# Kernel optimization log

Hardware: AMD Instinct MI355X
Metric: run time of the kernel (lower is better)

Reference implementation:

```python
import jax, jax.numpy as jnp
import numpy as np

K = 15          # n_clusters
D = 64          # dim_latent
M = 100         # number of w samples
LOG_2PI = float(np.log(2.0 * np.pi))

# state -> (cluster A, cluster B) edge endpoints, upper-triangular incl. diagonal
_A, _B = np.nonzero(np.triu(np.ones((K, K))))  # each [S], S = K*(K+1)/2 = 120


def setup_inputs() -> dict:
    key = jax.random.key(0)
    k1, k2, k3 = jax.random.split(key, 3)
    z = jax.random.normal(k1, (4096, 1, D), dtype=jnp.float32)      # [B, L, D]
    pi = jax.random.normal(k2, (1, K * (K + 1) // 2), dtype=jnp.float32)  # [1, S]
    mu = jax.random.uniform(k3, (D, K), dtype=jnp.float32, minval=-1.0, maxval=1.0)
    return {"z": z, "pi": pi, "mu": mu}


def reference(z, pi, mu):
    # w grid: [M]
    w = jnp.arange(M, dtype=z.dtype) / M
    # interpolated component means mu_sm[d, s, m] = mu[d,A[s]]*w[m] + mu[d,B[s]]*(1-w[m])
    mu_sm = mu[:, _A, None] * w + mu[:, _B, None] * (1.0 - w)   # [D, S, M]
    log_pi = jnp.log(jax.nn.softmax(pi, axis=-1) + 1e-30)       # [1, S]

    # squared distance via ||z||^2 - 2 z.mu + ||mu||^2 (avoids [B,L,D,S,M] materialization)
    zz = jnp.sum(z * z, axis=-1)                                # [B, L]
    cross = jnp.einsum('bld,dsm->blsm', z, mu_sm)               # [B, L, S, M]
    mm = jnp.sum(mu_sm * mu_sm, axis=0)                         # [S, M]
    sq = zz[..., None, None] - 2.0 * cross + mm                 # [B, L, S, M]

    log_p_zc_w = (-0.5 * D * LOG_2PI
                  + log_pi[0][None, None, :, None]
                  - 0.5 * sq)                                   # [B, L, S, M]
    log_p_z_L = jax.scipy.special.logsumexp(log_p_zc_w, axis=(2, 3))  # [B, L]
    log_p_z = jnp.mean(log_p_z_L) - jnp.log(jnp.asarray(M, z.dtype))
    return log_p_z
```

## Files before the change

### kernel.cpp

```cpp
#include <hip/hip_runtime.h>
#include <math.h>
#include <float.h>

#define D 64
#define K 15
#define S 120
#define MNUM 100
#define C0 (-58.81206612509905f)
#define L2E 1.4426950408889634f
#define INV_L2E 0.6931471805599453f
#define LOGM 4.605170185988091f

static __device__ __forceinline__ float fexp2(float x) {
    return __builtin_amdgcn_exp2f(x);
}

__global__ __launch_bounds__(256) void gmm_fused(const float* __restrict__ z,
                                                 const float* __restrict__ pi,
                                                 const float* __restrict__ mu,
                                                 float* __restrict__ out) {
    __shared__ float mush[D * K];
    __shared__ float G0[S], G1[S], G2[S];
    __shared__ unsigned char iA[S], iB[S];
    __shared__ float zsh[4][D];
    __shared__ float red[4];
    __shared__ float bsum[4];

    const int t = threadIdx.x;
    const int lane = t & 63;
    const int wv = t >> 6;

    for (int i = t; i < D * K; i += 256) mush[i] = mu[i];

    float p = (t < S) ? pi[t] : -FLT_MAX;
    float mx = p;
    #pragma unroll
    for (int off = 32; off; off >>= 1) mx = fmaxf(mx, __shfl_xor(mx, off));
    if (lane == 0) red[wv] = mx;
    __syncthreads();
    mx = fmaxf(fmaxf(red[0], red[1]), fmaxf(red[2], red[3]));

    float e = (t < S) ? __expf(p - mx) : 0.f;
    float se = e;
    #pragma unroll
    for (int off = 32; off; off >>= 1) se += __shfl_xor(se, off);
    __syncthreads();
    if (lane == 0) red[wv] = se;
    __syncthreads();
    se = red[0] + red[1] + red[2] + red[3];

    if (t < S) {
        float sm = e / se;
        float logpi = logf(sm + 1e-30f);

        int i = 0, rem = t;
        while (rem >= K - i) { rem -= K - i; ++i; }
        int j = i + rem;

        float aa = 0.f, ab = 0.f, bb = 0.f;
        #pragma unroll 8
        for (int d = 0; d < D; ++d) {
            float ma = mush[d * K + i];
            float mb = mush[d * K + j];
            aa = fmaf(ma, ma, aa);
            ab = fmaf(ma, mb, ab);
            bb = fmaf(mb, mb, bb);
        }
        float q0 = bb;
        float q1 = 2.f * (ab - bb);
        float q2 = aa - 2.f * ab + bb;

        G0[t] = C0 + logpi - 0.5f * q0;
        G1[t] = -0.5f * q1;
        G2[t] = -0.5f * q2;
        iA[t] = (unsigned char)i;
        iB[t] = (unsigned char)j;
    }

    const int b = (blockIdx.x << 2) + wv;
    float zval = z[b * D + lane];
    zsh[wv][lane] = zval;
    float zz = zval * zval;
    #pragma unroll
    for (int off = 32; off; off >>= 1) zz += __shfl_xor(zz, off);
    __syncthreads();

    const int g = lane >> 4;
    const int kk = lane & 15;
    const int kkc = (kk < K) ? kk : (K - 1);
    const float* zw = &zsh[wv][g * 16];
    float cpart = 0.f;
    #pragma unroll
    for (int i = 0; i < 16; ++i)
        cpart = fmaf(zw[i], mush[(g * 16 + i) * K + kkc], cpart);
    cpart += __shfl_xor(cpart, 16);
    cpart += __shfl_xor(cpart, 32);

    const int s1 = lane;
    const int s2 = lane + 64;
    const bool v2 = (s2 < S);
    const int s2c = v2 ? s2 : (S - 1);

    float cA1 = __shfl(cpart, (int)iA[s1]);
    float cB1 = __shfl(cpart, (int)iB[s1]);
    float cA2 = __shfl(cpart, (int)iA[s2c]);
    float cB2 = __shfl(cpart, (int)iB[s2c]);

    float T01 = G0[s1] + cB1 - 0.5f * zz;
    float T11 = G1[s1] + (cA1 - cB1);
    float T21 = G2[s1];
    float T02 = v2 ? (G0[s2c] + cB2 - 0.5f * zz) : -1e30f;
    float T12 = G1[s2c] + (cA2 - cB2);
    float T22 = G2[s2c];

    float bnd = fmaxf(T01, fmaf(0.99f, fmaf(0.99f, T21, T11), T01));
    if (T21 < 0.f) {
        float wv1 = fminf(fmaxf(-T11 * 0.5f * __builtin_amdgcn_rcpf(T21), 0.f), 0.99f);
        bnd = fmaxf(bnd, fmaf(wv1, fmaf(wv1, T21, T11), T01));
    }
    if (v2) {
        float b2 = fmaxf(T02, fmaf(0.99f, fmaf(0.99f, T22, T12), T02));
        if (T22 < 0.f) {
            float wv2 = fminf(fmaxf(-T12 * 0.5f * __builtin_amdgcn_rcpf(T22), 0.f), 0.99f);
            b2 = fmaxf(b2, fmaf(wv2, fmaf(wv2, T22, T12), T02));
        }
        bnd = fmaxf(bnd, b2);
    }
    #pragma unroll
    for (int off = 32; off; off >>= 1) bnd = fmaxf(bnd, __shfl_xor(bnd, off));
    const float Mb = bnd;

    const float a01 = (T01 - Mb) * L2E, a11 = T11 * L2E, a21 = T21 * L2E;
    const float a02 = (T02 - Mb) * L2E, a12 = T12 * L2E, a22 = T22 * L2E;

    float e1  = fexp2(fmaf(0.5f, fmaf(0.5f, a21, a11), a01));
    float g1  = fexp2(fmaf(0.0101f, a21,  0.01f * a11));
    float dd1 = fexp2(fmaf(-0.0099f, a21, -0.01f * a11));
    float h1  = fexp2(2.0e-4f * a21);

    float e2  = fexp2(fmaf(0.5f, fmaf(0.5f, a22, a12), a02));
    float g2  = fexp2(fmaf(0.0101f, a22,  0.01f * a12));
    float dd2 = fexp2(fmaf(-0.0099f, a22, -0.01f * a12));
    float h2  = fexp2(2.0e-4f * a22);

    float eu1 = e1,        gu1 = g1;
    float ed1 = e1 * dd1,  du1 = dd1 * h1;
    float eu2 = e2,        gu2 = g2;
    float ed2 = e2 * dd2,  du2 = dd2 * h2;
    float su1 = 0.f, sd1 = 0.f, su2 = 0.f, sd2 = 0.f;

    #pragma unroll 10
    for (int m = 0; m < 50; ++m) {
        su1 += eu1; eu1 *= gu1; gu1 *= h1;
        sd1 += ed1; ed1 *= du1; du1 *= h1;
        su2 += eu2; eu2 *= gu2; gu2 *= h2;
        sd2 += ed2; ed2 *= du2; du2 *= h2;
    }

    float ssum = (su1 + sd1) + (su2 + sd2);
    #pragma unroll
    for (int off = 32; off; off >>= 1) ssum += __shfl_xor(ssum, off);

    if (lane == 0)
        bsum[wv] = Mb + __builtin_amdgcn_logf(ssum) * INV_L2E;
    __syncthreads();
    if (t == 0) {
        float blk = ((bsum[0] + bsum[1]) + (bsum[2] + bsum[3]) - 4.f * LOGM)
                    * (1.0f / 4096.0f);
        atomicAdd(out, blk);
    }
}

extern "C" void kernel_launch(void* const* d_in, const int* in_sizes, int n_in,
                              void* d_out, int out_size, void* d_ws, size_t ws_size,
                              hipStream_t stream) {
    const float* z  = (const float*)d_in[0];
    const float* pi = (const float*)d_in[1];
    const float* mu = (const float*)d_in[2];
    float* out = (float*)d_out;

    hipMemsetAsync(out, 0, sizeof(float), stream);
    gmm_fused<<<1024, 256, 0, stream>>>(z, pi, mu, out);
}
```

Baseline: 75.99 us.

## Process two batch rows per wavefront and halve grid size

```diff
diff --git a/kernel.cpp b/kernel.cpp
--- a/kernel.cpp
+++ b/kernel.cpp
@@ -11,8 +11,16 @@
 #define INV_L2E 0.6931471805599453f
 #define LOGM 4.605170185988091f
 
-static __device__ __forceinline__ float fexp2(float x) {
-    return __builtin_amdgcn_exp2f(x);
+static __device__ __forceinline__ float fexp2(float x) { return __builtin_amdgcn_exp2f(x); }
+static __device__ __forceinline__ float flog2(float x) { return __builtin_amdgcn_logf(x); }
+
+static __device__ __forceinline__ float qbound(float T0, float T1, float T2, float r2) {
+    float bnd = fmaxf(T0, fmaf(0.99f, fmaf(0.99f, T2, T1), T0));
+    if (T2 < 0.f) {
+        float wx = fminf(fmaxf(-T1 * 0.5f * r2, 0.f), 0.99f);
+        bnd = fmaxf(bnd, fmaf(wx, fmaf(wx, T2, T1), T0));
+    }
+    return bnd;
 }
 
 __global__ __launch_bounds__(256) void gmm_fused(const float* __restrict__ z,
@@ -21,152 +29,182 @@
                                                  float* __restrict__ out) {
     __shared__ float mush[D * K];
     __shared__ float G0[S], G1[S], G2[S];
-    __shared__ unsigned char iA[S], iB[S];
-    __shared__ float zsh[4][D];
-    __shared__ float red[4];
-    __shared__ float bsum[4];
+    __shared__ int   iA[S], iB[S];
+    __shared__ float zsh[8][D];
+    __shared__ float bsum[8];
 
     const int t = threadIdx.x;
     const int lane = t & 63;
     const int wv = t >> 6;
+    const int b0 = (blockIdx.x << 3) + (wv << 1);
+
+    float zv0 = z[b0 * D + lane];
+    float zv1 = z[b0 * D + D + lane];
 
     for (int i = t; i < D * K; i += 256) mush[i] = mu[i];
 
-    float p = (t < S) ? pi[t] : -FLT_MAX;
-    float mx = p;
-    #pragma unroll
-    for (int off = 32; off; off >>= 1) mx = fmaxf(mx, __shfl_xor(mx, off));
-    if (lane == 0) red[wv] = mx;
+    zsh[(wv << 1)][lane] = zv0;
+    zsh[(wv << 1) + 1][lane] = zv1;
+    float zz0 = zv0 * zv0, zz1 = zv1 * zv1;
+    #pragma unroll
+    for (int off = 32; off; off >>= 1) {
+        zz0 += __shfl_xor(zz0, off);
+        zz1 += __shfl_xor(zz1, off);
+    }
+
     __syncthreads();
-    mx = fmaxf(fmaxf(red[0], red[1]), fmaxf(red[2], red[3]));
-
-    float e = (t < S) ? __expf(p - mx) : 0.f;
-    float se = e;
-    #pragma unroll
-    for (int off = 32; off; off >>= 1) se += __shfl_xor(se, off);
+
+    if (t < 128) {
+        float pa = pi[lane];
+        float pb = (lane < S - 64) ? pi[lane + 64] : -FLT_MAX;
+        float mx = fmaxf(pa, pb);
+        #pragma unroll
+        for (int off = 32; off; off >>= 1) mx = fmaxf(mx, __shfl_xor(mx, off));
+        float ea = fexp2((pa - mx) * L2E);
+        float eb = (lane < S - 64) ? fexp2((pb - mx) * L2E) : 0.f;
+        float se = ea + eb;
+        #pragma unroll
+        for (int off = 32; off; off >>= 1) se += __shfl_xor(se, off);
+
+        if (t < S) {
+            float e = wv ? eb : ea;
+            float logpi = logf(e / se + 1e-30f);
+
+            int i = 0, rem = t;
+            while (rem >= K - i) { rem -= K - i; ++i; }
+            int j = i + rem;
+
+            float aa = 0.f, ab = 0.f, bb = 0.f;
+            #pragma unroll 8
+            for (int d = 0; d < D; ++d) {
+                float ma = mush[d * K + i];
+                float mb = mush[d * K + j];
+                aa = fmaf(ma, ma, aa);
+                ab = fmaf(ma, mb, ab);
+                bb = fmaf(mb, mb, bb);
+            }
+            float q0 = bb;
+            float q1 = 2.f * (ab - bb);
+            float q2 = aa - 2.f * ab + bb;
+
+            G0[t] = C0 + logpi - 0.5f * q0;
+            G1[t] = -0.5f * q1;
+            G2[t] = -0.5f * q2;
+            iA[t] = i;
+            iB[t] = j;
+        }
+    }
     __syncthreads();
-    if (lane == 0) red[wv] = se;
-    __syncthreads();
-    se = red[0] + red[1] + red[2] + red[3];
-
-    if (t < S) {
-        float sm = e / se;
-        float logpi = logf(sm + 1e-30f);
-
-        int i = 0, rem = t;
-        while (rem >= K - i) { rem -= K - i; ++i; }
-        int j = i + rem;
-
-        float aa = 0.f, ab = 0.f, bb = 0.f;
-        #pragma unroll 8
-        for (int d = 0; d < D; ++d) {
-            float ma = mush[d * K + i];
-            float mb = mush[d * K + j];
-            aa = fmaf(ma, ma, aa);
-            ab = fmaf(ma, mb, ab);
-            bb = fmaf(mb, mb, bb);
-        }
-        float q0 = bb;
-        float q1 = 2.f * (ab - bb);
-        float q2 = aa - 2.f * ab + bb;
-
-        G0[t] = C0 + logpi - 0.5f * q0;
-        G1[t] = -0.5f * q1;
-        G2[t] = -0.5f * q2;
-        iA[t] = (unsigned char)i;
-        iB[t] = (unsigned char)j;
-    }
-
-    const int b = (blockIdx.x << 2) + wv;
-    float zval = z[b * D + lane];
-    zsh[wv][lane] = zval;
-    float zz = zval * zval;
-    #pragma unroll
-    for (int off = 32; off; off >>= 1) zz += __shfl_xor(zz, off);
-    __syncthreads();
-
-    const int g = lane >> 4;
+
+    const int grp = lane >> 4;
     const int kk = lane & 15;
     const int kkc = (kk < K) ? kk : (K - 1);
-    const float* zw = &zsh[wv][g * 16];
-    float cpart = 0.f;
-    #pragma unroll
-    for (int i = 0; i < 16; ++i)
-        cpart = fmaf(zw[i], mush[(g * 16 + i) * K + kkc], cpart);
-    cpart += __shfl_xor(cpart, 16);
-    cpart += __shfl_xor(cpart, 32);
+    const float* zw0 = &zsh[(wv << 1)][grp * 16];
+    const float* zw1 = &zsh[(wv << 1) + 1][grp * 16];
+    float c0 = 0.f, c1 = 0.f;
+    #pragma unroll
+    for (int i = 0; i < 16; ++i) {
+        float m = mush[(grp * 16 + i) * K + kkc];
+        c0 = fmaf(zw0[i], m, c0);
+        c1 = fmaf(zw1[i], m, c1);
+    }
+    c0 += __shfl_xor(c0, 16); c0 += __shfl_xor(c0, 32);
+    c1 += __shfl_xor(c1, 16); c1 += __shfl_xor(c1, 32);
 
     const int s1 = lane;
     const int s2 = lane + 64;
     const bool v2 = (s2 < S);
     const int s2c = v2 ? s2 : (S - 1);
 
-    float cA1 = __shfl(cpart, (int)iA[s1]);
-    float cB1 = __shfl(cpart, (int)iB[s1]);
-    float cA2 = __shfl(cpart, (int)iA[s2c]);
-    float cB2 = __shfl(cpart, (int)iB[s2c]);
-
-    float T01 = G0[s1] + cB1 - 0.5f * zz;
-    float T11 = G1[s1] + (cA1 - cB1);
-    float T21 = G2[s1];
-    float T02 = v2 ? (G0[s2c] + cB2 - 0.5f * zz) : -1e30f;
-    float T12 = G1[s2c] + (cA2 - cB2);
-    float T22 = G2[s2c];
-
-    float bnd = fmaxf(T01, fmaf(0.99f, fmaf(0.99f, T21, T11), T01));
-    if (T21 < 0.f) {
-        float wv1 = fminf(fmaxf(-T11 * 0.5f * __builtin_amdgcn_rcpf(T21), 0.f), 0.99f);
-        bnd = fmaxf(bnd, fmaf(wv1, fmaf(wv1, T21, T11), T01));
-    }
-    if (v2) {
-        float b2 = fmaxf(T02, fmaf(0.99f, fmaf(0.99f, T22, T12), T02));
-        if (T22 < 0.f) {
-            float wv2 = fminf(fmaxf(-T12 * 0.5f * __builtin_amdgcn_rcpf(T22), 0.f), 0.99f);
-            b2 = fmaxf(b2, fmaf(wv2, fmaf(wv2, T22, T12), T02));
-        }
-        bnd = fmaxf(bnd, b2);
-    }
-    #pragma unroll
-    for (int off = 32; off; off >>= 1) bnd = fmaxf(bnd, __shfl_xor(bnd, off));
-    const float Mb = bnd;
-
-    const float a01 = (T01 - Mb) * L2E, a11 = T11 * L2E, a21 = T21 * L2E;
-    const float a02 = (T02 - Mb) * L2E, a12 = T12 * L2E, a22 = T22 * L2E;
-
-    float e1  = fexp2(fmaf(0.5f, fmaf(0.5f, a21, a11), a01));
-    float g1  = fexp2(fmaf(0.0101f, a21,  0.01f * a11));
-    float dd1 = fexp2(fmaf(-0.0099f, a21, -0.01f * a11));
-    float h1  = fexp2(2.0e-4f * a21);
-
-    float e2  = fexp2(fmaf(0.5f, fmaf(0.5f, a22, a12), a02));
-    float g2  = fexp2(fmaf(0.0101f, a22,  0.01f * a12));
-    float dd2 = fexp2(fmaf(-0.0099f, a22, -0.01f * a12));
-    float h2  = fexp2(2.0e-4f * a22);
-
-    float eu1 = e1,        gu1 = g1;
-    float ed1 = e1 * dd1,  du1 = dd1 * h1;
-    float eu2 = e2,        gu2 = g2;
-    float ed2 = e2 * dd2,  du2 = dd2 * h2;
-    float su1 = 0.f, sd1 = 0.f, su2 = 0.f, sd2 = 0.f;
+    const int ia1 = iA[s1], ib1 = iB[s1];
+    const int ia2 = iA[s2c], ib2 = iB[s2c];
+    const float g01 = G0[s1], g11 = G1[s1], T21 = G2[s1];
+    const float g02 = G0[s2c], g12 = G1[s2c], T22 = G2[s2c];
+
+    float cA10 = __shfl(c0, ia1), cB10 = __shfl(c0, ib1);
+    float cA20 = __shfl(c0, ia2), cB20 = __shfl(c0, ib2);
+    float cA11 = __shfl(c1, ia1), cB11 = __shfl(c1, ib1);
+    float cA21 = __shfl(c1, ia2), cB21 = __shfl(c1, ib2);
+
+    float T010 = g01 + cB10 - 0.5f * zz0;
+    float T110 = g11 + (cA10 - cB10);
+    float T020 = v2 ? (g02 + cB20 - 0.5f * zz0) : -1e30f;
+    float T120 = g12 + (cA20 - cB20);
+    float T011 = g01 + cB11 - 0.5f * zz1;
+    float T111 = g11 + (cA11 - cB11);
+    float T021 = v2 ? (g02 + cB21 - 0.5f * zz1) : -1e30f;
+    float T121 = g12 + (cA21 - cB21);
+
+    const float r21 = __builtin_amdgcn_rcpf(T21);
+    const float r22 = __builtin_amdgcn_rcpf(T22);
+
+    float bnd0 = fmaxf(qbound(T010, T110, T21, r21), qbound(T020, T120, T22, r22));
+    float bnd1 = fmaxf(qbound(T011, T111, T21, r21), qbound(T021, T121, T22, r22));
+    #pragma unroll
+    for (int off = 32; off; off >>= 1) {
+        bnd0 = fmaxf(bnd0, __shfl_xor(bnd0, off));
+        bnd1 = fmaxf(bnd1, __shfl_xor(bnd1, off));
+    }
+    const float Mb0 = bnd0, Mb1 = bnd1;
+
+    const float a2_1 = T21 * L2E, a2_2 = T22 * L2E;
+    const float a0_10 = (T010 - Mb0) * L2E, a1_10 = T110 * L2E;
+    const float a0_20 = (T020 - Mb0) * L2E, a1_20 = T120 * L2E;
+    const float a0_11 = (T011 - Mb1) * L2E, a1_11 = T111 * L2E;
+    const float a0_21 = (T021 - Mb1) * L2E, a1_21 = T121 * L2E;
+
+    const float h1 = fexp2(2.0e-4f * a2_1);
+    const float h2 = fexp2(2.0e-4f * a2_2);
+
+    float e10 = fexp2(fmaf(0.5f, fmaf(0.5f, a2_1, a1_10), a0_10));
+    float g10 = fexp2(fmaf(0.0101f, a2_1,  0.01f * a1_10));
+    float d10 = fexp2(fmaf(-0.0099f, a2_1, -0.01f * a1_10));
+    float e20 = fexp2(fmaf(0.5f, fmaf(0.5f, a2_2, a1_20), a0_20));
+    float g20 = fexp2(fmaf(0.0101f, a2_2,  0.01f * a1_20));
+    float d20 = fexp2(fmaf(-0.0099f, a2_2, -0.01f * a1_20));
+    float e11 = fexp2(fmaf(0.5f, fmaf(0.5f, a2_1, a1_11), a0_11));
+    float g11x = fexp2(fmaf(0.0101f, a2_1,  0.01f * a1_11));
+    float d11 = fexp2(fmaf(-0.0099f, a2_1, -0.01f * a1_11));
+    float e21 = fexp2(fmaf(0.5f, fmaf(0.5f, a2_2, a1_21), a0_21));
+    float g21x = fexp2(fmaf(0.0101f, a2_2,  0.01f * a1_21));
+    float d21 = fexp2(fmaf(-0.0099f, a2_2, -0.01f * a1_21));
+
+    float eu10 = e10,       gu10 = g10,       ed10 = e10 * d10, du10 = d10 * h1;
+    float eu20 = e20,       gu20 = g20,       ed20 = e20 * d20, du20 = d20 * h2;
+    float eu11 = e11,       gu11 = g11x,      ed11 = e11 * d11, du11 = d11 * h1;
+    float eu21 = e21,       gu21 = g21x,      ed21 = e21 * d21, du21 = d21 * h2;
+    float su10 = 0.f, sd10 = 0.f, su20 = 0.f, sd20 = 0.f;
+    float su11 = 0.f, sd11 = 0.f, su21 = 0.f, sd21 = 0.f;
 
     #pragma unroll 10
     for (int m = 0; m < 50; ++m) {
-        su1 += eu1; eu1 *= gu1; gu1 *= h1;
-        sd1 += ed1; ed1 *= du1; du1 *= h1;
-        su2 += eu2; eu2 *= gu2; gu2 *= h2;
-        sd2 += ed2; ed2 *= du2; du2 *= h2;
-    }
-
-    float ssum = (su1 + sd1) + (su2 + sd2);
-    #pragma unroll
-    for (int off = 32; off; off >>= 1) ssum += __shfl_xor(ssum, off);
-
-    if (lane == 0)
-        bsum[wv] = Mb + __builtin_amdgcn_logf(ssum) * INV_L2E;
+        su10 += eu10; eu10 *= gu10; gu10 *= h1;
+        sd10 += ed10; ed10 *= du10; du10 *= h1;
+        su20 += eu20; eu20 *= gu20; gu20 *= h2;
+        sd20 += ed20; ed20 *= du20; du20 *= h2;
+        su11 += eu11; eu11 *= gu11; gu11 *= h1;
+        sd11 += ed11; ed11 *= du11; du11 *= h1;
+        su21 += eu21; eu21 *= gu21; gu21 *= h2;
+        sd21 += ed21; ed21 *= du21; du21 *= h2;
+    }
+
+    float ssum0 = (su10 + sd10) + (su20 + sd20);
+    float ssum1 = (su11 + sd11) + (su21 + sd21);
+    #pragma unroll
+    for (int off = 32; off; off >>= 1) {
+        ssum0 += __shfl_xor(ssum0, off);
+        ssum1 += __shfl_xor(ssum1, off);
+    }
+
+    if (lane == 0) {
+        bsum[(wv << 1)]     = Mb0 + flog2(ssum0) * INV_L2E;
+        bsum[(wv << 1) + 1] = Mb1 + flog2(ssum1) * INV_L2E;
+    }
     __syncthreads();
     if (t == 0) {
-        float blk = ((bsum[0] + bsum[1]) + (bsum[2] + bsum[3]) - 4.f * LOGM)
-                    * (1.0f / 4096.0f);
+        float blk = (((bsum[0] + bsum[1]) + (bsum[2] + bsum[3]))
+                   + ((bsum[4] + bsum[5]) + (bsum[6] + bsum[7]))
+                   - 8.f * LOGM) * (1.0f / 4096.0f);
         atomicAdd(out, blk);
     }
 }
@@ -180,5 +218,5 @@
     float* out = (float*)d_out;
 
     hipMemsetAsync(out, 0, sizeof(float), stream);
-    gmm_fused<<<1024, 256, 0, stream>>>(z, pi, mu, out);
+    gmm_fused<<<512, 256, 0, stream>>>(z, pi, mu, out);
 }
```

Result: faster. 70.01 us (-7.9%).
